# Kernel optimization log

Measured on AMD Instinct MI355X. Metric: run time of the kernel, lower is better.

The kernel has to match this reference:

```python
import jax, jax.numpy as jnp
import numpy as np

B, N, D = 8, 1024, 1024
H, HD = 16, 64          # n_heads, head_dim = D // H
FF = 2 * D              # SwiGLU hidden dim (ffn_dim_mult=2)
EPS = 1e-5


def setup_inputs() -> dict:
    key = jax.random.key(0)
    ks = jax.random.split(key, 10)
    s = 0.02
    return {
        "x": jax.random.normal(ks[0], (B, N, D), dtype=jnp.float32),
        "attn_norm_scale": jnp.ones((D,), jnp.float32),
        "ffn_norm_scale": jnp.ones((D,), jnp.float32),
        "wq": jax.random.normal(ks[1], (D, D), jnp.float32) * s,
        "bq": jnp.zeros((D,), jnp.float32),
        "wk": jax.random.normal(ks[2], (D, D), jnp.float32) * s,
        "bk": jnp.zeros((D,), jnp.float32),
        "wv": jax.random.normal(ks[3], (D, D), jnp.float32) * s,
        "bv": jnp.zeros((D,), jnp.float32),
        "wo": jax.random.normal(ks[4], (D, D), jnp.float32) * s,
        "bo": jnp.zeros((D,), jnp.float32),
        "w_uv": jax.random.normal(ks[5], (D, 2 * FF), jnp.float32) * s,
        "w_out": jax.random.normal(ks[6], (FF, D), jnp.float32) * s,
    }


def _rmsnorm(x, scale):
    xf = x.astype(jnp.float32)
    y = xf * jax.lax.rsqrt(jnp.mean(xf * xf, axis=-1, keepdims=True) + EPS)
    return scale * y.astype(x.dtype)


def reference(x, attn_norm_scale, ffn_norm_scale, wq, bq, wk, bk, wv, bv,
              wo, bo, w_uv, w_out):
    # FFT2D: fft over channel dim then token dim, keep real part
    x = jnp.fft.fft(jnp.fft.fft(x, axis=-1), axis=-2).real.astype(jnp.float32)

    # --- self attention with pre-RMSNorm and residual ---
    xn = _rmsnorm(x, attn_norm_scale)
    q = (xn @ wq + bq).reshape(B, N, H, HD)
    k = (xn @ wk + bk).reshape(B, N, H, HD)
    v = (xn @ wv + bv).reshape(B, N, H, HD)
    scores = jnp.einsum('bnhd,bmhd->bhnm', q, k) / np.sqrt(HD).astype(np.float32)
    attn = jax.nn.softmax(scores, axis=-1)
    o = jnp.einsum('bhnm,bmhd->bnhd', attn, v).reshape(B, N, D)
    x = (o @ wo + bo) + x

    # --- SwiGLU FFN with pre-RMSNorm and residual ---
    xn = _rmsnorm(x, ffn_norm_scale)
    uv = xn @ w_uv                      # [B, N, 2*FF]
    u, vg = uv[..., :FF], uv[..., FF:]
    x = (jax.nn.silu(u) * vg) @ w_out + x
    return x
```

## Files before the change

### kernel.cpp

```cpp
#include <hip/hip_runtime.h>
#include <stdint.h>

typedef unsigned short u16;
typedef __attribute__((ext_vector_type(8))) __bf16 bf16x8;
typedef __attribute__((ext_vector_type(4))) float f32x4;
typedef __attribute__((ext_vector_type(8))) u16 u16x8;

static __device__ __forceinline__ u16 f2bf(float f){
  uint32_t x = __builtin_bit_cast(uint32_t, f);
  x = (x + 0x7FFFu + ((x >> 16) & 1u)) >> 16;
  return (u16)x;
}
static __device__ __forceinline__ u16 f2bf_fast(float f){
  uint32_t x = __builtin_bit_cast(uint32_t, f);
  return (u16)((x + 0x8000u) >> 16);
}
static __device__ __forceinline__ float bf2f(u16 h){
  uint32_t x = ((uint32_t)h) << 16;
  return __builtin_bit_cast(float, x);
}
static __device__ __forceinline__ f32x4 mfma16(bf16x8 a, bf16x8 b, f32x4 c){
  return __builtin_amdgcn_mfma_f32_16x16x32_bf16(a, b, c, 0, 0, 0);
}
static __device__ __forceinline__ void gload16(const void* g, void* l){
  __builtin_amdgcn_global_load_lds(
      (const __attribute__((address_space(1))) void*)(uintptr_t)g,
      (__attribute__((address_space(3))) void*)(uint32_t)(uintptr_t)l,
      16, 0, 0);
}

__global__ __launch_bounds__(256) void k_prep(
    const float* __restrict__ x,  const float* __restrict__ wq,
    const float* __restrict__ wk, const float* __restrict__ wv,
    const float* __restrict__ wo, const float* __restrict__ wuv,
    const float* __restrict__ wout,
    const float* __restrict__ bq, const float* __restrict__ bk,
    const float* __restrict__ bv,
    u16* __restrict__ Cb, u16* __restrict__ Sb,
    u16* __restrict__ xbFp, u16* __restrict__ xbFm,
    u16* __restrict__ wqkvt, u16* __restrict__ wot, u16* __restrict__ wuvt,
    u16* __restrict__ woutt, float* __restrict__ bqkv)
{
  int bid = blockIdx.x;
  int t = threadIdx.x;
  __shared__ float tl[32][33];
  __shared__ float tlB[32][33];
  if (bid < 1024){
    int n = bid, m0 = t * 4;
    #pragma unroll
    for (int i = 0; i < 4; ++i){
      int m = m0 + i;
      int ph = (n * m) & 1023;
      float a = (float)ph * (1.0f / 512.0f);
      int idx = n * 1024 + m;
      Cb[idx] = f2bf(cospif(a)); Sb[idx] = f2bf(sinpif(a));
    }
    return;
  }
  bid -= 1024;
  if (bid >= 15360){
    int i = (bid - 15360) * 256 + t;
    bqkv[i] = i < 1024 ? bq[i] : (i < 2048 ? bk[i - 1024] : bv[i - 2048]);
    return;
  }
  int lx = t & 31, ly = t >> 5;
  if (bid < 5120){
    int z = bid / 640, rem = bid % 640;
    int dt = rem >> 5, nt = rem & 31;
    int d0 = dt * 32, n0 = nt * 32;
    const float* ip = x + ((int64_t)z << 20);
    if (dt <= 16){
      #pragma unroll
      for (int k8 = 0; k8 < 32; k8 += 8)
        tl[ly + k8][lx] = ip[(int64_t)(n0 + ly + k8) * 1024 + d0 + lx];
    }
    if (dt <= 15){
      #pragma unroll
      for (int k8 = 0; k8 < 32; k8 += 8){
        float v = 0.0f;
        if (!(d0 == 0 && lx == 31))
          v = ip[(int64_t)(n0 + ly + k8) * 1024 + (993 - d0 + lx)];
        tlB[ly + k8][lx] = v;
      }
    }
    __syncthreads();
    u16* op = xbFp + (int64_t)z * 655360 + n0 + lx;
    u16* om = xbFm + (int64_t)z * 655360 + n0 + lx;
    #pragma unroll
    for (int k8 = 0; k8 < 32; k8 += 8){
      int i_ = ly + k8, dd = d0 + i_;
      float a = 0.f, m = 0.f;
      if (dt <= 15){
        a = tl[lx][i_];
        m = (dd == 0) ? 0.f : tlB[lx][31 - i_];
      } else if (dt == 16){
        a = (i_ == 0) ? tl[lx][0] : 0.f;
      }
      op[(int64_t)dd * 1024] = f2bf(a + m);
      om[(int64_t)dd * 1024] = f2bf(a - m);
    }
    return;
  }
  const float* in; u16* out; int Cc, R, bx, by;
  int64_t outOff = 0;
  bool uvperm = false;
  if (bid < 9216){
    int j = (bid - 5120) >> 10, tile = (bid - 5120) & 1023;
    const float* srcs[4] = {wq, wk, wv, wo};
    in = srcs[j]; Cc = 1024; R = 1024;
    if (j < 3){ out = wqkvt; outOff = (int64_t)j << 20; }
    else      { out = wot; }
    bx = tile & 31; by = tile >> 5;
  } else if (bid < 13312){
    int tile = bid - 9216;
    in = wuv; out = wuvt; Cc = 4096; R = 1024; uvperm = true;
    bx = tile & 127; by = tile >> 7;
  } else {
    int tile = bid - 13312;
    in = wout; out = woutt; Cc = 1024; R = 2048;
    bx = tile & 31; by = tile >> 5;
  }
  int tc = bx * 32, tr = by * 32;
  #pragma unroll
  for (int i = 0; i < 32; i += 8)
    tl[ly + i][lx] = in[(int64_t)(tr + ly + i) * Cc + tc + lx];
  __syncthreads();
  if (uvperm){
    #pragma unroll
    for (int i = 0; i < 32; i += 8){
      int c = tc + ly + i;
      int pr = (c < 2048) ? ((c >> 4) * 32 + (c & 15))
                          : (((c - 2048) >> 4) * 32 + 16 + ((c - 2048) & 15));
      out[(int64_t)pr * 1024 + tr + lx] = f2bf(tl[lx][ly + i]);
    }
  } else {
    u16* op = out + outOff;
    #pragma unroll
    for (int i = 0; i < 32; i += 8)
      op[(int64_t)(tc + ly + i) * R + tr + lx] = f2bf(tl[lx][ly + i]);
  }
}

__global__ __launch_bounds__(256) void k_rmsnorm(const float* __restrict__ x,
                                                 const float* __restrict__ sc,
                                                 u16* __restrict__ out){
  int r = blockIdx.x;
  const float4* px = (const float4*)(x + (int64_t)r * 1024);
  float4 v = px[threadIdx.x];
  float ss = v.x*v.x + v.y*v.y + v.z*v.z + v.w*v.w;
  #pragma unroll
  for (int o = 1; o < 64; o <<= 1) ss += __shfl_xor(ss, o);
  __shared__ float red[4];
  if ((threadIdx.x & 63) == 0) red[threadIdx.x >> 6] = ss;
  __syncthreads();
  float tot = red[0] + red[1] + red[2] + red[3];
  float rs = rsqrtf(tot * (1.0f / 1024.0f) + 1e-5f);
  float4 s4 = ((const float4*)sc)[threadIdx.x];
  ushort4 ov;
  ov.x = f2bf(v.x * rs * s4.x); ov.y = f2bf(v.y * rs * s4.y);
  ov.z = f2bf(v.z * rs * s4.z); ov.w = f2bf(v.w * rs * s4.w);
  ((ushort4*)(out + (int64_t)r * 1024))[threadIdx.x] = ov;
}

__global__ __launch_bounds__(256) void k_fftfin(const u16* __restrict__ Uw,
                                                const float* __restrict__ sc,
                                                float* __restrict__ Y,
                                                u16* __restrict__ xn){
  int row = blockIdx.x;
  int b = row >> 10, k = row & 1023;
  int kp = (k <= 512) ? k : 1024 - k;
  float sm = (k <= 512) ? 1.0f : -1.0f;
  const u16* ub = Uw + (int64_t)b * 819200 + (int64_t)kp * 640;
  const u16* wb = ub + 640 * 640;
  int c0 = threadIdx.x * 4;
  float y[4];
  #pragma unroll
  for (int i = 0; i < 4; ++i){
    int c = c0 + i;
    int tp = (c <= 512) ? c : 1024 - c;
    float st = (c <= 512) ? sm : -sm;
    y[i] = bf2f(ub[tp]) - st * bf2f(wb[tp]);
  }
  float ss = y[0]*y[0] + y[1]*y[1] + y[2]*y[2] + y[3]*y[3];
  #pragma unroll
  for (int o = 1; o < 64; o <<= 1) ss += __shfl_xor(ss, o);
  __shared__ float red[4];
  if ((threadIdx.x & 63) == 0) red[threadIdx.x >> 6] = ss;
  __syncthreads();
  float tot = red[0] + red[1] + red[2] + red[3];
  float rs = rsqrtf(tot * (1.0f / 1024.0f) + 1e-5f);
  float4 s4 = ((const float4*)sc)[threadIdx.x];
  float4 yo; yo.x = y[0]; yo.y = y[1]; yo.z = y[2]; yo.w = y[3];
  ((float4*)(Y + (int64_t)row * 1024))[threadIdx.x] = yo;
  ushort4 ov;
  ov.x = f2bf(y[0] * rs * s4.x); ov.y = f2bf(y[1] * rs * s4.y);
  ov.z = f2bf(y[2] * rs * s4.z); ov.w = f2bf(y[3] * rs * s4.w);
  ((ushort4*)(xn + (int64_t)row * 1024))[threadIdx.x] = ov;
}

template<int MR, bool SILU, bool COLCHUNK>
__global__ __launch_bounds__(256, (MR == 8) ? 2 : 4) void k_gemm4(
    const u16* __restrict__ A0, const u16* __restrict__ A1,
    const u16* __restrict__ B0, const u16* __restrict__ B1,
    void* Cout, const float* __restrict__ bias, const float* resid,
    u16* __restrict__ vtbuf, int vtn0,
    int nkt, int rowSplit, int lda, int ldb, int ldc,
    int64_t aB, int64_t bB, int64_t cB, int outBf16)
{
  constexpr int BM = MR * 32;
  constexpr int ABUF = BM * 64;
  constexpr int BUFB = ABUF + 8192;
  constexpr int APASS = ABUF / 4096;
  __shared__ char smem[2 * BUFB];

  int z = blockIdx.z;
  int nwg = gridDim.x * gridDim.y;
  int bid = blockIdx.y * gridDim.x + blockIdx.x;
  int q = nwg >> 3, r = nwg & 7, xc = bid & 7, off = bid >> 3;
  int sw = (xc < r ? xc * (q + 1) : r * (q + 1) + (xc - r) * q) + off;
  int bx, by;
  if (COLCHUNK){
    bx = sw / gridDim.y; by = sw % gridDim.y;
  } else {
    int gx = gridDim.x;
    int GW = ((gx & 15) == 0) ? 16 : (((gx & 7) == 0) ? 8 : gx);
    int gsz = GW * gridDim.y;
    int grp = sw / gsz, rem = sw % gsz;
    bx = grp * GW + rem % GW;
    by = rem / GW;
  }

  int tm = by * BM, tn = bx * 128;
  int tid = threadIdx.x;
  int lane = tid & 63, w = tid >> 6;
  int lr = lane & 15, lg = lane >> 4;
  int wOffM = (w >> 1) * (BM / 2), wOffN = (w & 1) * 64;

  const u16* Ap = ((tm < rowSplit) ? A0 : A1) + (int64_t)z * aB;
  const u16* Bp = ((tm < rowSplit) ? B0 : B1) + (int64_t)z * bB;
  int64_t cOff = (int64_t)z * cB;

  const u16* pA[APASS];
  const u16* pB[2];
  #pragma unroll
  for (int p = 0; p < APASS; ++p){
    int D = tid * 16 + p * 4096, line = D >> 7, sp = ((D >> 4) & 7) ^ (line & 7);
    int rr = line * 2 + (sp >> 2), kg = sp & 3;
    pA[p] = Ap + (int64_t)(tm + rr) * lda + kg * 8;
  }
  #pragma unroll
  for (int p = 0; p < 2; ++p){
    int D = tid * 16 + p * 4096, line = D >> 7, sp = ((D >> 4) & 7) ^ (line & 7);
    int rr = line * 2 + (sp >> 2), kg = sp & 3;
    pB[p] = Bp + (int64_t)(tn + rr) * ldb + kg * 8;
  }

  int slotR = (lg + ((lr & 1) << 2)) ^ ((lr >> 1) & 7);
  int aRB = ((wOffM >> 1) + (lr >> 1)) * 128 + slotR * 16;
  int bRB = ((wOffN >> 1) + (lr >> 1)) * 128 + slotR * 16;

  const f32x4 fz = {0.f, 0.f, 0.f, 0.f};
  f32x4 acc[MR][4];
  #pragma unroll
  for (int i = 0; i < MR; ++i)
    #pragma unroll
    for (int j = 0; j < 4; ++j) acc[i][j] = fz;

  auto STAGE = [&](int kt, int bf){
    int k0 = kt * 32;
    char* d = smem + bf * BUFB + tid * 16;
    #pragma unroll
    for (int p = 0; p < APASS; ++p) gload16(pA[p] + k0, d + p * 4096);
    #pragma unroll
    for (int p = 0; p < 2; ++p) gload16(pB[p] + k0, d + ABUF + p * 4096);
  };
  auto COMPUTE = [&](const char* Ab){
    const char* Bb = Ab + ABUF;
    bf16x8 af[MR], bfr[4];
    #pragma unroll
    for (int i = 0; i < MR; ++i) af[i] = *(const bf16x8*)(Ab + aRB + i * 1024);
    #pragma unroll
    for (int j = 0; j < 4; ++j) bfr[j] = *(const bf16x8*)(Bb + bRB + j * 1024);
    #pragma unroll
    for (int i = 0; i < MR; ++i)
      #pragma unroll
      for (int j = 0; j < 4; ++j)
        acc[i][j] = mfma16(af[i], bfr[j], acc[i][j]);
  };

  STAGE(0, 0);
  __syncthreads();
  for (int kt = 0; kt < nkt; kt += 2){
    STAGE(kt + 1, 1);
    COMPUTE(smem);
    __syncthreads();
    if (kt + 2 < nkt) STAGE(kt + 2, 0);
    COMPUTE(smem + BUFB);
    __syncthreads();
  }

  if constexpr (SILU){
    int colBase = ((tn + wOffN) >> 1) + lr;
    #pragma unroll
    for (int i = 0; i < MR; ++i){
      #pragma unroll
      for (int jj = 0; jj < 4; ++jj){
        int row = tm + wOffM + i * 16 + lg * 4 + jj;
        #pragma unroll
        for (int jp = 0; jp < 2; ++jp){
          float u = acc[i][jp * 2][jj], v = acc[i][jp * 2 + 1][jj];
          float s = u / (1.0f + __expf(-u));
          ((u16*)Cout)[(int64_t)row * ldc + colBase + jp * 16] = f2bf(s * v);
        }
      }
    }
    return;
  }
  if (vtbuf && tn >= vtn0){
    int b = tm >> 10;
    int key0 = (tm & 1023) + wOffM + lg * 4;
    #pragma unroll
    for (int j = 0; j < 4; ++j){
      int col = tn + wOffN + j * 16 + lr;
      int hv = (col - 2048) >> 6, d = (col - 2048) & 63;
      float badd = bias ? bias[col] : 0.0f;
      u16* vb = vtbuf + ((int64_t)(b * 16 + hv) << 16) + d * 1024;
      #pragma unroll
      for (int i = 0; i < MR; ++i){
        ushort4 pk;
        pk.x = f2bf(acc[i][j][0] + badd);
        pk.y = f2bf(acc[i][j][1] + badd);
        pk.z = f2bf(acc[i][j][2] + badd);
        pk.w = f2bf(acc[i][j][3] + badd);
        *(ushort4*)(vb + key0 + i * 16) = pk;
      }
    }
    return;
  }
  #pragma unroll
  for (int i = 0; i < MR; ++i){
    #pragma unroll
    for (int j = 0; j < 4; ++j){
      int col = tn + wOffN + j * 16 + lr;
      float badd = bias ? bias[col] : 0.0f;
      #pragma unroll
      for (int jj = 0; jj < 4; ++jj){
        int row = tm + wOffM + i * 16 + lg * 4 + jj;
        int64_t idx = cOff + (int64_t)row * ldc + col;
        float v = acc[i][j][jj] + badd;
        if (resid) v += resid[idx];
        if (outBf16) ((u16*)Cout)[idx] = f2bf(v);
        else         ((float*)Cout)[idx] = v;
      }
    }
  }
}

__global__ __launch_bounds__(512, 4) void k_attn2(const u16* __restrict__ qkv,
                                                  const u16* __restrict__ vt,
                                                  u16* __restrict__ O){
  __shared__ u16 Ks[2][4096];
  __shared__ u16 Vts[2][4096];
  __shared__ u16 Pl[8][2304];
  int bh = blockIdx.y; int b = bh >> 4, h = bh & 15;
  int qt = blockIdx.x;
  int t = threadIdx.x, w = t >> 6, lane = t & 63, lr = lane & 15, lg = lane >> 4;
  int sr = t >> 3, sl = t & 7;
  int swz = (sl ^ (sr & 7)) * 8;

  const u16* kg = qkv + (int64_t)b * 1024 * 3072 + 1024 + h * 64;
  const u16* vg = vt + (int64_t)bh * 65536;

  const u16* qrow = qkv + (int64_t)(b * 1024 + qt * 256 + w * 32 + lr) * 3072 + h * 64;
  bf16x8 aq[2][2];
  #pragma unroll
  for (int m = 0; m < 2; ++m)
    #pragma unroll
    for (int kc = 0; kc < 2; ++kc)
      aq[m][kc] = *(const bf16x8*)(qrow + (int64_t)m * 16 * 3072 + kc * 32 + lg * 8);

  const f32x4 fz = {0.f, 0.f, 0.f, 0.f};
  f32x4 o_[2][4];
  float lj[2][4];
  #pragma unroll
  for (int m = 0; m < 2; ++m){
    #pragma unroll
    for (int d = 0; d < 4; ++d) o_[m][d] = fz;
    #pragma unroll
    for (int j = 0; j < 4; ++j) lj[m][j] = 0.f;
  }

  #define STAGE(ktile, bn) do {                                                   \
    gload16(kg + (int64_t)((ktile) * 64 + sr) * 3072 + swz,                       \
            (char*)Ks + (bn) * 8192 + t * 16);                                    \
    gload16(vg + (int64_t)sr * 1024 + (ktile) * 64 + swz,                         \
            (char*)Vts + (bn) * 8192 + t * 16);                                   \
  } while (0)

  STAGE(0, 0);
  __syncthreads();
  int buf = 0;
  int lsw = lr & 7;

  const float CSC = 0.1803368801111204f;
  const float MSH = 8.656170245333781f;

  #pragma unroll 1
  for (int kt = 0; kt < 16; ++kt){
    if (kt < 15) STAGE(kt + 1, buf ^ 1);

    f32x4 s[2][4];
    #pragma unroll
    for (int m = 0; m < 2; ++m)
      #pragma unroll
      for (int n = 0; n < 4; ++n) s[m][n] = fz;
    #pragma unroll
    for (int n = 0; n < 4; ++n){
      #pragma unroll
      for (int kc = 0; kc < 2; ++kc){
        bf16x8 kb = *(const bf16x8*)&Ks[buf][(n * 16 + lr) * 64 + (((kc * 4 + lg) ^ lsw) * 8)];
        s[0][n] = mfma16(aq[0][kc], kb, s[0][n]);
        s[1][n] = mfma16(aq[1][kc], kb, s[1][n]);
      }
    }

    #pragma unroll
    for (int m = 0; m < 2; ++m){
      #pragma unroll
      for (int j = 0; j < 4; ++j){
        float p0 = exp2f(fmaf(s[m][0][j], CSC, -MSH));
        float p1 = exp2f(fmaf(s[m][1][j], CSC, -MSH));
        float p2 = exp2f(fmaf(s[m][2][j], CSC, -MSH));
        float p3 = exp2f(fmaf(s[m][3][j], CSC, -MSH));
        lj[m][j] += (p0 + p1) + (p2 + p3);
        u16* pb = &Pl[w][(m * 16 + lg * 4 + j) * 72 + lr];
        pb[0]  = f2bf_fast(p0); pb[16] = f2bf_fast(p1);
        pb[32] = f2bf_fast(p2); pb[48] = f2bf_fast(p3);
      }
    }
    asm volatile("s_waitcnt lgkmcnt(0)" ::: "memory");
    __builtin_amdgcn_sched_barrier(0);

    #pragma unroll
    for (int kc = 0; kc < 2; ++kc){
      bf16x8 pa0 = *(const bf16x8*)&Pl[w][(lr) * 72 + kc * 32 + lg * 8];
      bf16x8 pa1 = *(const bf16x8*)&Pl[w][(16 + lr) * 72 + kc * 32 + lg * 8];
      #pragma unroll
      for (int dt = 0; dt < 4; ++dt){
        bf16x8 vb = *(const bf16x8*)&Vts[buf][(dt * 16 + lr) * 64 + (((kc * 4 + lg) ^ lsw) * 8)];
        o_[0][dt] = mfma16(pa0, vb, o_[0][dt]);
        o_[1][dt] = mfma16(pa1, vb, o_[1][dt]);
      }
    }
    __syncthreads();
    buf ^= 1;
  }
  #undef STAGE

  u16* obase = O + (int64_t)(b * 1024 + qt * 256 + w * 32) * 1024 + h * 64;
  #pragma unroll
  for (int m = 0; m < 2; ++m){
    #pragma unroll
    for (int j = 0; j < 4; ++j){
      float l = lj[m][j];
      l += __shfl_xor(l, 1); l += __shfl_xor(l, 2);
      l += __shfl_xor(l, 4); l += __shfl_xor(l, 8);
      float inv = 1.0f / l;
      int q = m * 16 + lg * 4 + j;
      #pragma unroll
      for (int dt = 0; dt < 4; ++dt)
        obase[(int64_t)q * 1024 + dt * 16 + lr] = f2bf(o_[m][dt][j] * inv);
    }
  }
}

extern "C" void kernel_launch(void* const* d_in, const int* in_sizes, int n_in,
                              void* d_out, int out_size, void* d_ws, size_t ws_size,
                              hipStream_t stream)
{
  (void)in_sizes; (void)n_in; (void)out_size; (void)ws_size;
  const float* x    = (const float*)d_in[0];
  const float* ans  = (const float*)d_in[1];
  const float* fns  = (const float*)d_in[2];
  const float* wq   = (const float*)d_in[3];
  const float* bq   = (const float*)d_in[4];
  const float* wk   = (const float*)d_in[5];
  const float* bk   = (const float*)d_in[6];
  const float* wv   = (const float*)d_in[7];
  const float* bvv  = (const float*)d_in[8];
  const float* wo   = (const float*)d_in[9];
  const float* bo   = (const float*)d_in[10];
  const float* wuv  = (const float*)d_in[11];
  const float* wout = (const float*)d_in[12];

  char* ws = (char*)d_ws;
  const size_t MB = 1u << 20;
  const int64_t XBF = 655360;
  const int64_t FB2 = (int64_t)1280 * 640;
  const int BIG = 1 << 30;
  u16*  xbFp  = (u16*)(ws + 0 * MB);
  u16*  xbFm  = (u16*)(ws + 11 * MB);
  u16*  Xcs   = (u16*)(ws + 22 * MB);
  u16*  Uw    = (u16*)(ws + 36 * MB);
  u16*  xn    = (u16*)(ws + 56 * MB);
  u16*  qkv   = (u16*)(ws + 0 * MB);
  u16*  vtg   = (u16*)(ws + 72 * MB);
  u16*  Obuf  = (u16*)(ws + 88 * MB);
  u16*  xn2   = (u16*)(ws + 0 * MB);
  u16*  g     = (u16*)(ws + 16 * MB);
  u16*  Cb    = (u16*)(ws + 104 * MB);
  u16*  Sb    = (u16*)(ws + 106 * MB);
  u16*  wqkvt = (u16*)(ws + 108 * MB);
  u16*  wot   = (u16*)(ws + 114 * MB);
  u16*  wuvt  = (u16*)(ws + 116 * MB);
  u16*  woutt = (u16*)(ws + 124 * MB);
  float* bqkv = (float*)(ws + 128 * MB);
  float* outF = (float*)d_out;

  k_prep<<<dim3(16396), 256, 0, stream>>>(x, wq, wk, wv, wo, wuv, wout,
      bq, bk, bvv, Cb, Sb, xbFp, xbFm, wqkvt, wot, wuvt, woutt, bqkv);

  k_gemm4<4, false, true><<<dim3(5, 10, 8), 256, 0, stream>>>(
      Cb, Sb - 640 * 1024, xbFp, xbFm, Xcs, nullptr, nullptr, nullptr, BIG,
      32, 640, 1024, 1024, 640, 0, XBF, FB2, 1);
  k_gemm4<4, false, false><<<dim3(5, 10, 8), 256, 0, stream>>>(
      Xcs, Xcs, Cb, Sb, Uw, nullptr, nullptr, nullptr, BIG,
      20, 640, 640, 1024, 640, FB2, 0, FB2, 1);
  k_fftfin<<<dim3(8192), 256, 0, stream>>>(Uw, ans, outF, xn);

  k_gemm4<4, false, false><<<dim3(24, 64, 1), 256, 0, stream>>>(
      xn, xn, wqkvt, wqkvt, qkv, bqkv, nullptr, vtg, 2048,
      32, BIG, 1024, 1024, 3072, 0, 0, 0, 1);
  k_attn2<<<dim3(4, 128), 512, 0, stream>>>(qkv, vtg, Obuf);
  k_gemm4<4, false, false><<<dim3(8, 64, 1), 256, 0, stream>>>(
      Obuf, Obuf, wot, wot, d_out, bo, outF, nullptr, BIG,
      32, BIG, 1024, 1024, 1024, 0, 0, 0, 0);

  k_rmsnorm<<<dim3(8192), 256, 0, stream>>>(outF, fns, xn2);
  k_gemm4<8, true, false><<<dim3(32, 32, 1), 256, 0, stream>>>(
      xn2, xn2, wuvt, wuvt, g, nullptr, nullptr, nullptr, BIG,
      32, BIG, 1024, 1024, 2048, 0, 0, 0, 1);
  k_gemm4<4, false, false><<<dim3(8, 64, 1), 256, 0, stream>>>(
      g, g, woutt, woutt, d_out, nullptr, outF, nullptr, BIG,
      64, BIG, 2048, 2048, 1024, 0, 0, 0, 0);
}
```

Measured before the change: 379.8 us.

## Fold token-axis symmetry into FFT prep to halve first DFT GEMM K

The prep kernel now folds the input along both the channel and token axes, combining the four mirrored quadrants into even/odd symmetric sums. This shrinks the first DFT GEMM's reduction length from 1024 to 640 (20 K-tiles instead of 32) and its input buffers to 640x640 per batch. The cost is four tile loads per prep block and more index logic, and the symmetric folding has to reproduce the real-part FFT semantics exactly.

Result: no change. 376.9 us (median of 2 runs) (-0.8%).

```diff
diff --git a/kernel.cpp b/kernel.cpp
--- a/kernel.cpp
+++ b/kernel.cpp
@@ -37,14 +37,16 @@
     const float* __restrict__ bq, const float* __restrict__ bk,
     const float* __restrict__ bv,
     u16* __restrict__ Cb, u16* __restrict__ Sb,
-    u16* __restrict__ xbFp, u16* __restrict__ xbFm,
+    u16* __restrict__ xP, u16* __restrict__ xM,
     u16* __restrict__ wqkvt, u16* __restrict__ wot, u16* __restrict__ wuvt,
     u16* __restrict__ woutt, float* __restrict__ bqkv)
 {
   int bid = blockIdx.x;
   int t = threadIdx.x;
-  __shared__ float tl[32][33];
-  __shared__ float tlB[32][33];
+  __shared__ float tA[32][33];
+  __shared__ float tB[32][33];
+  __shared__ float tC[32][33];
+  __shared__ float tD[32][33];
   if (bid < 1024){
     int n = bid, m0 = t * 4;
     #pragma unroll
@@ -58,72 +60,90 @@
     return;
   }
   bid -= 1024;
-  if (bid >= 15360){
-    int i = (bid - 15360) * 256 + t;
+  if (bid >= 13440){
+    int i = (bid - 13440) * 256 + t;
     bqkv[i] = i < 1024 ? bq[i] : (i < 2048 ? bk[i - 1024] : bv[i - 2048]);
     return;
   }
   int lx = t & 31, ly = t >> 5;
-  if (bid < 5120){
-    int z = bid / 640, rem = bid % 640;
-    int dt = rem >> 5, nt = rem & 31;
+  if (bid < 3200){
+    int z = bid / 400, rem = bid % 400;
+    int dt = rem / 20, nt = rem % 20;
     int d0 = dt * 32, n0 = nt * 32;
     const float* ip = x + ((int64_t)z << 20);
-    if (dt <= 16){
-      #pragma unroll
-      for (int k8 = 0; k8 < 32; k8 += 8)
-        tl[ly + k8][lx] = ip[(int64_t)(n0 + ly + k8) * 1024 + d0 + lx];
-    }
+    #pragma unroll
+    for (int k8 = 0; k8 < 32; k8 += 8)
+      tA[ly + k8][lx] = ip[(int64_t)(n0 + ly + k8) * 1024 + d0 + lx];
     if (dt <= 15){
       #pragma unroll
       for (int k8 = 0; k8 < 32; k8 += 8){
-        float v = 0.0f;
+        float v = 0.f;
         if (!(d0 == 0 && lx == 31))
           v = ip[(int64_t)(n0 + ly + k8) * 1024 + (993 - d0 + lx)];
-        tlB[ly + k8][lx] = v;
+        tB[ly + k8][lx] = v;
+      }
+    }
+    if (nt <= 15){
+      #pragma unroll
+      for (int k8 = 0; k8 < 32; k8 += 8){
+        float v = 0.f;
+        if (!(n0 == 0 && (ly + k8) == 31))
+          v = ip[(int64_t)(993 - n0 + ly + k8) * 1024 + d0 + lx];
+        tC[ly + k8][lx] = v;
+      }
+    }
+    if (dt <= 15 && nt <= 15){
+      #pragma unroll
+      for (int k8 = 0; k8 < 32; k8 += 8){
+        float v = 0.f;
+        if (!(n0 == 0 && (ly + k8) == 31) && !(d0 == 0 && lx == 31))
+          v = ip[(int64_t)(993 - n0 + ly + k8) * 1024 + (993 - d0 + lx)];
+        tD[ly + k8][lx] = v;
       }
     }
     __syncthreads();
-    u16* op = xbFp + (int64_t)z * 655360 + n0 + lx;
-    u16* om = xbFm + (int64_t)z * 655360 + n0 + lx;
+    u16* Pp = xP + (int64_t)z * 409600 + n0 + lx;
+    u16* Mp = xM + (int64_t)z * 409600 + n0 + lx;
     #pragma unroll
     for (int k8 = 0; k8 < 32; k8 += 8){
-      int i_ = ly + k8, dd = d0 + i_;
-      float a = 0.f, m = 0.f;
-      if (dt <= 15){
-        a = tl[lx][i_];
-        m = (dd == 0) ? 0.f : tlB[lx][31 - i_];
-      } else if (dt == 16){
-        a = (i_ == 0) ? tl[lx][0] : 0.f;
-      }
-      op[(int64_t)dd * 1024] = f2bf(a + m);
-      om[(int64_t)dd * 1024] = f2bf(a - m);
+      int dj = ly + k8;
+      int d = d0 + dj, n = n0 + lx;
+      bool dv = (d >= 1 && d <= 511), nv = (n >= 1 && n <= 511);
+      float base = tA[lx][dj];
+      float dm = dv ? tB[lx][31 - dj] : 0.f;
+      float nm = nv ? tC[31 - lx][dj] : 0.f;
+      float bm = (dv && nv) ? tD[31 - lx][31 - dj] : 0.f;
+      float pv = base + dm + nm + bm;
+      float mv = base - dm - nm + bm;
+      if (d > 512 || n > 512){ pv = 0.f; mv = 0.f; }
+      Pp[(int64_t)d * 640] = f2bf(pv);
+      Mp[(int64_t)d * 640] = f2bf(mv);
     }
     return;
   }
   const float* in; u16* out; int Cc, R, bx, by;
   int64_t outOff = 0;
   bool uvperm = false;
-  if (bid < 9216){
-    int j = (bid - 5120) >> 10, tile = (bid - 5120) & 1023;
+  if (bid < 7296){
+    int j = (bid - 3200) >> 10, tile = (bid - 3200) & 1023;
     const float* srcs[4] = {wq, wk, wv, wo};
     in = srcs[j]; Cc = 1024; R = 1024;
     if (j < 3){ out = wqkvt; outOff = (int64_t)j << 20; }
     else      { out = wot; }
     bx = tile & 31; by = tile >> 5;
-  } else if (bid < 13312){
-    int tile = bid - 9216;
+  } else if (bid < 11392){
+    int tile = bid - 7296;
     in = wuv; out = wuvt; Cc = 4096; R = 1024; uvperm = true;
     bx = tile & 127; by = tile >> 7;
   } else {
-    int tile = bid - 13312;
+    int tile = bid - 11392;
     in = wout; out = woutt; Cc = 1024; R = 2048;
     bx = tile & 31; by = tile >> 5;
   }
   int tc = bx * 32, tr = by * 32;
   #pragma unroll
   for (int i = 0; i < 32; i += 8)
-    tl[ly + i][lx] = in[(int64_t)(tr + ly + i) * Cc + tc + lx];
+    tA[ly + i][lx] = in[(int64_t)(tr + ly + i) * Cc + tc + lx];
   __syncthreads();
   if (uvperm){
     #pragma unroll
@@ -131,13 +151,13 @@
       int c = tc + ly + i;
       int pr = (c < 2048) ? ((c >> 4) * 32 + (c & 15))
                           : (((c - 2048) >> 4) * 32 + 16 + ((c - 2048) & 15));
-      out[(int64_t)pr * 1024 + tr + lx] = f2bf(tl[lx][ly + i]);
+      out[(int64_t)pr * 1024 + tr + lx] = f2bf(tA[lx][ly + i]);
     }
   } else {
     u16* op = out + outOff;
     #pragma unroll
     for (int i = 0; i < 32; i += 8)
-      op[(int64_t)(tc + ly + i) * R + tr + lx] = f2bf(tl[lx][ly + i]);
+      op[(int64_t)(tc + ly + i) * R + tr + lx] = f2bf(tA[lx][ly + i]);
   }
 }
 
@@ -495,13 +515,13 @@
 
   char* ws = (char*)d_ws;
   const size_t MB = 1u << 20;
-  const int64_t XBF = 655360;
+  const int64_t XPB = 409600;
   const int64_t FB2 = (int64_t)1280 * 640;
   const int BIG = 1 << 30;
-  u16*  xbFp  = (u16*)(ws + 0 * MB);
-  u16*  xbFm  = (u16*)(ws + 11 * MB);
-  u16*  Xcs   = (u16*)(ws + 22 * MB);
-  u16*  Uw    = (u16*)(ws + 36 * MB);
+  u16*  xP    = (u16*)(ws + 0 * MB);
+  u16*  xM    = (u16*)(ws + 7 * MB);
+  u16*  Xcs   = (u16*)(ws + 14 * MB);
+  u16*  Uw    = (u16*)(ws + 28 * MB);
   u16*  xn    = (u16*)(ws + 56 * MB);
   u16*  qkv   = (u16*)(ws + 0 * MB);
   u16*  vtg   = (u16*)(ws + 72 * MB);
@@ -517,12 +537,12 @@
   float* bqkv = (float*)(ws + 128 * MB);
   float* outF = (float*)d_out;
 
-  k_prep<<<dim3(16396), 256, 0, stream>>>(x, wq, wk, wv, wo, wuv, wout,
-      bq, bk, bvv, Cb, Sb, xbFp, xbFm, wqkvt, wot, wuvt, woutt, bqkv);
+  k_prep<<<dim3(14476), 256, 0, stream>>>(x, wq, wk, wv, wo, wuv, wout,
+      bq, bk, bvv, Cb, Sb, xP, xM, wqkvt, wot, wuvt, woutt, bqkv);
 
   k_gemm4<4, false, true><<<dim3(5, 10, 8), 256, 0, stream>>>(
-      Cb, Sb - 640 * 1024, xbFp, xbFm, Xcs, nullptr, nullptr, nullptr, BIG,
-      32, 640, 1024, 1024, 640, 0, XBF, FB2, 1);
+      Cb, Sb - 640 * 1024, xP, xM, Xcs, nullptr, nullptr, nullptr, BIG,
+      20, 640, 1024, 640, 640, 0, XPB, FB2, 1);
   k_gemm4<4, false, false><<<dim3(5, 10, 8), 256, 0, stream>>>(
       Xcs, Xcs, Cb, Sb, Uw, nullptr, nullptr, nullptr, BIG,
       20, 640, 640, 1024, 640, FB2, 0, FB2, 1);
```
